# Kernel optimization log

Measured on AMD Instinct MI355X. Metric: run time of the kernel, lower is better.

## Reference

```python
import jax, jax.numpy as jnp
import numpy as np

B = 1024           # number of drug pairs (graphs per side)
ATOMS = 64         # atoms per molecule
N = B * ATOMS      # total atoms per side
H = 512            # hidden_size * number_of_molecules
FFN_H = 2048
OUT = 86           # num_tasks


def setup_inputs() -> dict:
    key = jax.random.key(0)
    ks = jax.random.split(key, 12)
    inv = 1.0 / np.sqrt(H)
    inv2 = 1.0 / np.sqrt(2 * H)
    invf = 1.0 / np.sqrt(FFN_H)
    return {
        "left_output": jax.random.normal(ks[0], (B, H), jnp.float32),
        "right_output": jax.random.normal(ks[1], (B, H), jnp.float32),
        "left_atom": jax.random.normal(ks[2], (N, H), jnp.float32),
        "right_atom": jax.random.normal(ks[3], (N, H), jnp.float32),
        "left_batch": jnp.arange(N, dtype=jnp.int32) // ATOMS,
        "right_batch": jnp.arange(N, dtype=jnp.int32) // ATOMS,
        "noise": jax.random.uniform(ks[4], (B, H), jnp.float32),
        "w_i_w": jax.random.normal(ks[5], (H, H), jnp.float32) * inv,
        "w_i_b": jnp.zeros((H,), jnp.float32),
        "prj_i_w": jax.random.normal(ks[6], (H, H), jnp.float32) * inv,
        "prj_i_b": jnp.zeros((H,), jnp.float32),
        "ffn1_w": jax.random.normal(ks[7], (2 * H, FFN_H), jnp.float32) * inv2,
        "ffn1_b": jnp.zeros((FFN_H,), jnp.float32),
        "ffn2_w": jax.random.normal(ks[8], (FFN_H, OUT), jnp.float32) * invf,
        "ffn2_b": jnp.zeros((OUT,), jnp.float32),
    }


def _seg_softmax(s, seg, num_segments):
    m = jax.ops.segment_max(s, seg, num_segments=num_segments)
    e = jnp.exp(s - m[seg])
    z = jax.ops.segment_sum(e, seg, num_segments=num_segments)
    return e / z[seg]


def reference(left_output, right_output, left_atom, right_atom,
              left_batch, right_batch, noise,
              w_i_w, w_i_b, prj_i_w, prj_i_b,
              ffn1_w, ffn1_b, ffn2_w, ffn2_b):
    # repeat_interleave(left_output, degree(right_batch)) == gather by segment id
    left_align = left_output[right_batch]    # [N_r, H]
    right_align = right_output[left_batch]   # [N_l, H]

    # cross-molecule coattention scores (elementwise product + reduce)
    left_scores = jnp.sum((left_atom @ w_i_w + w_i_b) * (right_align @ prj_i_w + prj_i_b), axis=-1)
    left_scores = _seg_softmax(left_scores, left_batch, B)
    right_scores = jnp.sum((right_atom @ w_i_w + w_i_b) * (left_align @ prj_i_w + prj_i_b), axis=-1)
    right_scores = _seg_softmax(right_scores, right_batch, B)

    # attention-weighted global add pool
    h_output = jax.ops.segment_sum(left_atom * right_align * left_scores[:, None], left_batch, num_segments=B)
    t_output = jax.ops.segment_sum(right_atom * left_align * right_scores[:, None], right_batch, num_segments=B)

    # sign-directed noise perturbation (same noise for both sides, as in original)
    nrm = jnp.maximum(jnp.linalg.norm(noise, axis=-1, keepdims=True), 1e-12)
    noise_n = noise / nrm
    h_pert = h_output + jnp.sign(h_output) * noise_n * 0.1
    t_pert = t_output + jnp.sign(t_output) * noise_n * 0.1

    pair = jnp.concatenate([h_pert, t_pert], axis=-1)  # [B, 2H]
    hid = jax.nn.relu(pair @ ffn1_w + ffn1_b)
    output = hid @ ffn2_w + ffn2_b  # training mode: raw logits, no sigmoid
    return (output, h_output, h_pert, left_scores, right_scores, left_output, right_output)
```

## Files before the change

kernel.cpp:

```cpp
#include <hip/hip_runtime.h>
#include <hip/hip_bf16.h>
#include <float.h>

#define B_ 1024
#define H_ 512
#define N_ (B_ * 64)
#define FFN_ 2048
#define OUT_ 86

typedef __bf16 bf16_t;
typedef __attribute__((ext_vector_type(8))) __bf16 bf16x8;
typedef __attribute__((ext_vector_type(4))) float f32x4;

__device__ __forceinline__ float wred_sum(float v) {
#pragma unroll
  for (int m = 32; m; m >>= 1) v += __shfl_xor(v, m);
  return v;
}

__device__ __forceinline__ void gload_lds16(const void* g, void* l) {
  __builtin_amdgcn_global_load_lds((const __attribute__((address_space(1))) unsigned int*)g,
                                   (__attribute__((address_space(3))) unsigned int*)l, 16, 0, 0);
}

__global__ void k_prep(const float* __restrict__ w_i_b,
                       const float* __restrict__ prj_w, const float* __restrict__ prj_b,
                       float* __restrict__ ev, float* __restrict__ c0) {
  int b = blockIdx.x, l = threadIdx.x;
  float s = 0.f;
  if (b < 512) {
    for (int h = l; h < H_; h += 64) s += prj_w[b * H_ + h] * w_i_b[h];
    s = wred_sum(s);
    if (l == 0) ev[b] = s;
  } else {
    for (int h = l; h < H_; h += 64) s += w_i_b[h] * prj_b[h];
    s = wred_sum(s);
    if (l == 0) c0[0] = s;
  }
}

__global__ void k_cvec(const float* __restrict__ ro, const float* __restrict__ lo,
                       const float* __restrict__ ev, const float* __restrict__ c0,
                       float* __restrict__ cL, float* __restrict__ cR) {
  int b = blockIdx.x, side = blockIdx.y, l = threadIdx.x;
  const float* x = side ? lo : ro;
  float s = 0.f;
  for (int j = l; j < H_; j += 64) s += x[b * H_ + j] * ev[j];
  s = wred_sum(s);
  if (l == 0) (side ? cR : cL)[b] = s + c0[0];
}

template <bool BT, bool BIAS>
__global__ __launch_bounds__(256) void gemm64(const float* __restrict__ A1, const float* __restrict__ A2,
                                              int M1, const float* __restrict__ Bm,
                                              const float* __restrict__ bias, float* __restrict__ C,
                                              int N, int K) {
  __shared__ float As[16][68];
  __shared__ float Bs[16][68];
  const int bm = blockIdx.x * 64, bn = blockIdx.y * 64;
  const float* __restrict__ A = (bm < M1) ? (A1 + (size_t)bm * K) : (A2 + (size_t)(bm - M1) * K);
  const int t = threadIdx.x;
  const int tx = t & 15, ty = t >> 4;
  float acc[4][4] = {};
  for (int k0 = 0; k0 < K; k0 += 16) {
#pragma unroll
    for (int i = 0; i < 4; i++) {
      int m = (t >> 4) + i * 16;
      As[t & 15][m] = A[(size_t)m * K + k0 + (t & 15)];
    }
    if (BT) {
#pragma unroll
      for (int i = 0; i < 4; i++) {
        int n = (t >> 4) + i * 16;
        Bs[t & 15][n] = Bm[(size_t)(bn + n) * K + k0 + (t & 15)];
      }
    } else {
#pragma unroll
      for (int i = 0; i < 4; i++) {
        int kk = (t >> 6) + i * 4;
        Bs[kk][t & 63] = Bm[(size_t)(k0 + kk) * N + bn + (t & 63)];
      }
    }
    __syncthreads();
#pragma unroll
    for (int kk = 0; kk < 16; kk++) {
      float4 av = *(const float4*)&As[kk][ty * 4];
      float4 bv = *(const float4*)&Bs[kk][tx * 4];
      float a_[4] = {av.x, av.y, av.z, av.w};
      float b_[4] = {bv.x, bv.y, bv.z, bv.w};
#pragma unroll
      for (int i = 0; i < 4; i++)
#pragma unroll
        for (int j = 0; j < 4; j++) acc[i][j] += a_[i] * b_[j];
    }
    __syncthreads();
  }
#pragma unroll
  for (int i = 0; i < 4; i++) {
    int m = bm + ty * 4 + i;
    float tmp[4];
#pragma unroll
    for (int j = 0; j < 4; j++) {
      float x = acc[i][j];
      if (BIAS) x += bias[bn + tx * 4 + j];
      tmp[j] = x;
    }
    float4 v;
    v.x = tmp[0]; v.y = tmp[1]; v.z = tmp[2]; v.w = tmp[3];
    *(float4*)&C[(size_t)m * N + bn + tx * 4] = v;
  }
}

__global__ __launch_bounds__(256, 2) void k_atoms2(const float* __restrict__ atomL, const float* __restrict__ atomR,
                                                   const float* __restrict__ uLR,
                                                   const float* __restrict__ cL, const float* __restrict__ cR,
                                                   float* __restrict__ scoresL, float* __restrict__ scoresR,
                                                   float* __restrict__ pL, float* __restrict__ pR) {
  const int gw = blockIdx.x * 4 + (threadIdx.x >> 6);
  const int side = gw >> 10;
  const int b = gw & 1023;
  const int lane = threadIdx.x & 63;

  const float* __restrict__ atom = side ? atomR : atomL;
  const float cb = (side ? cR : cL)[b];
  float* __restrict__ scores = side ? scoresR : scoresL;
  float* __restrict__ p = side ? pR : pL;

  const float* __restrict__ u = uLR + (size_t)gw * H_;
  float ur[8];
  *(f32x4*)&ur[0] = *(const f32x4*)&u[lane * 8];
  *(f32x4*)&ur[4] = *(const f32x4*)&u[lane * 8 + 4];

  const float* __restrict__ base = atom + (size_t)b * 64 * H_ + lane * 8;

  float q[8] = {};
  float m_run = -FLT_MAX, z_run = 0.f;
  float myraw = 0.f;

#pragma unroll
  for (int c = 0; c < 8; c++) {
    float a[8][8];
#pragma unroll
    for (int i = 0; i < 8; i++) {
      const float* rp = base + (size_t)(c * 8 + i) * H_;
      *(f32x4*)&a[i][0] = *(const f32x4*)rp;
      *(f32x4*)&a[i][4] = *(const f32x4*)(rp + 4);
    }
    float d[8];
#pragma unroll
    for (int i = 0; i < 8; i++) {
      float s = 0.f;
#pragma unroll
      for (int j = 0; j < 8; j++) s += a[i][j] * ur[j];
      d[i] = s;
    }
#pragma unroll
    for (int i = 0; i < 8; i++) d[i] = wred_sum(d[i]) + cb;
#pragma unroll
    for (int i = 0; i < 8; i++) myraw = (lane == c * 8 + i) ? d[i] : myraw;
    float mc = d[0];
#pragma unroll
    for (int i = 1; i < 8; i++) mc = fmaxf(mc, d[i]);
    float m_new = fmaxf(m_run, mc);
    float r = __expf(m_run - m_new);
    float e[8];
    float zc = 0.f;
#pragma unroll
    for (int i = 0; i < 8; i++) { e[i] = __expf(d[i] - m_new); zc += e[i]; }
    z_run = z_run * r + zc;
    m_run = m_new;
#pragma unroll
    for (int j = 0; j < 8; j++) q[j] *= r;
#pragma unroll
    for (int i = 0; i < 8; i++)
#pragma unroll
      for (int j = 0; j < 8; j++) q[j] += e[i] * a[i][j];
  }

  const float zinv = 1.f / z_run;
  float outp[8];
#pragma unroll
  for (int j = 0; j < 8; j++) outp[j] = q[j] * zinv;
  float* pd = p + (size_t)b * H_ + lane * 8;
  *(f32x4*)&pd[0] = *(const f32x4*)&outp[0];
  *(f32x4*)&pd[4] = *(const f32x4*)&outp[4];
  scores[(size_t)b * 64 + lane] = __expf(myraw - m_run) * zinv;
}

__global__ __launch_bounds__(512) void k_pert(const float* __restrict__ lo, const float* __restrict__ ro,
                                              const float* __restrict__ noise,
                                              const float* __restrict__ pL, const float* __restrict__ pR,
                                              float* __restrict__ h_out, float* __restrict__ h_pert,
                                              bf16_t* __restrict__ pairbf) {
  const int b = blockIdx.x, t = threadIdx.x;
  float nv = noise[(size_t)b * H_ + t];
  float sq = nv * nv;
  sq = wred_sum(sq);
  __shared__ float red[8];
  if ((t & 63) == 0) red[t >> 6] = sq;
  __syncthreads();
  float tot = 0.f;
#pragma unroll
  for (int i = 0; i < 8; i++) tot += red[i];
  float nrm = fmaxf(sqrtf(tot), 1e-12f);
  float nn = nv / nrm * 0.1f;
  float h = ro[(size_t)b * H_ + t] * pL[(size_t)b * H_ + t];
  float tt = lo[(size_t)b * H_ + t] * pR[(size_t)b * H_ + t];
  float sh = (h > 0.f) ? 1.f : ((h < 0.f) ? -1.f : 0.f);
  float st = (tt > 0.f) ? 1.f : ((tt < 0.f) ? -1.f : 0.f);
  float hp = h + sh * nn;
  float tp = tt + st * nn;
  h_out[(size_t)b * H_ + t] = h;
  h_pert[(size_t)b * H_ + t] = hp;
  pairbf[(size_t)b * 1024 + t] = (bf16_t)hp;
  pairbf[(size_t)b * 1024 + 512 + t] = (bf16_t)tp;
}

__global__ __launch_bounds__(256) void k_w1t(const float* __restrict__ W1, bf16_t* __restrict__ W1t) {
  __shared__ float tile[32][33];
  const int bx = blockIdx.x;
  const int by = blockIdx.y;
  const int tx = threadIdx.x & 31, ty = threadIdx.x >> 5;
#pragma unroll
  for (int i = ty; i < 32; i += 8)
    tile[i][tx] = W1[(size_t)(by * 32 + i) * FFN_ + bx * 32 + tx];
  __syncthreads();
#pragma unroll
  for (int i = ty; i < 32; i += 8)
    W1t[(size_t)(bx * 32 + i) * 1024 + by * 32 + tx] = (bf16_t)tile[tx][i];
}

__global__ __launch_bounds__(256) void k_ffn1(const bf16_t* __restrict__ Abf, const bf16_t* __restrict__ Bt,
                                              const float* __restrict__ bias, float* __restrict__ C) {
  __shared__ bf16_t As[64 * 64];
  __shared__ bf16_t Bs[64 * 64];
  const int bm = blockIdx.x * 64, bn = blockIdx.y * 64;
  const int t = threadIdx.x;
  const int lane = t & 63, wave = t >> 6;
  const int wm = wave & 1, wn = wave >> 1;
  const int l15 = lane & 15, l4 = lane >> 4;
  f32x4 acc[2][2] = {{{0.f, 0.f, 0.f, 0.f}, {0.f, 0.f, 0.f, 0.f}},
                     {{0.f, 0.f, 0.f, 0.f}, {0.f, 0.f, 0.f, 0.f}}};

  for (int k0 = 0; k0 < 1024; k0 += 64) {
#pragma unroll
    for (int r = 0; r < 2; r++) {
      const int off = (r * 256 + t) * 16;
      const int row = off >> 7;
      const int g = (off >> 4) & 7;
      const int scb = ((g ^ (row & 7)) << 4);
      gload_lds16((const char*)Abf + (size_t)(bm + row) * 2048 + k0 * 2 + scb, (char*)As + off);
      gload_lds16((const char*)Bt + (size_t)(bn + row) * 2048 + k0 * 2 + scb, (char*)Bs + off);
    }
    __syncthreads();
#pragma unroll
    for (int ks = 0; ks < 2; ks++) {
      const int ar0 = wm * 32 + l15, ar1 = ar0 + 16;
      const int br0 = wn * 32 + l15, br1 = br0 + 16;
      const int gA = ks * 4 + l4;
      bf16x8 a0 = *(const bf16x8*)((const char*)As + ar0 * 128 + ((gA ^ (ar0 & 7)) << 4));
      bf16x8 a1 = *(const bf16x8*)((const char*)As + ar1 * 128 + ((gA ^ (ar1 & 7)) << 4));
      bf16x8 b0 = *(const bf16x8*)((const char*)Bs + br0 * 128 + ((gA ^ (br0 & 7)) << 4));
      bf16x8 b1 = *(const bf16x8*)((const char*)Bs + br1 * 128 + ((gA ^ (br1 & 7)) << 4));
      acc[0][0] = __builtin_amdgcn_mfma_f32_16x16x32_bf16(a0, b0, acc[0][0], 0, 0, 0);
      acc[0][1] = __builtin_amdgcn_mfma_f32_16x16x32_bf16(a0, b1, acc[0][1], 0, 0, 0);
      acc[1][0] = __builtin_amdgcn_mfma_f32_16x16x32_bf16(a1, b0, acc[1][0], 0, 0, 0);
      acc[1][1] = __builtin_amdgcn_mfma_f32_16x16x32_bf16(a1, b1, acc[1][1], 0, 0, 0);
    }
    __syncthreads();
  }
#pragma unroll
  for (int mi = 0; mi < 2; mi++)
#pragma unroll
    for (int nj = 0; nj < 2; nj++)
#pragma unroll
      for (int r = 0; r < 4; r++) {
        const int m = bm + wm * 32 + mi * 16 + l4 * 4 + r;
        const int n = bn + wn * 32 + nj * 16 + l15;
        float v = acc[mi][nj][r] + bias[n];
        C[(size_t)m * FFN_ + n] = fmaxf(v, 0.f);
      }
}

__global__ void k_w2t(const float* __restrict__ W2, float* __restrict__ W2t) {
  int idx = blockIdx.x * 256 + threadIdx.x;
  if (idx < OUT_ * FFN_) {
    int n = idx / FFN_, k = idx % FFN_;
    W2t[idx] = W2[(size_t)k * OUT_ + n];
  }
}

__global__ __launch_bounds__(256) void k_ffn2(const float* __restrict__ hid, const float* __restrict__ W2t,
                                              const float* __restrict__ b2, float* __restrict__ out) {
  const int b0 = blockIdx.x * 2;
  const int t = threadIdx.x, wave = t >> 6, lane = t & 63;
  float4 h0[8], h1[8];
  const float* r0 = hid + (size_t)b0 * FFN_;
#pragma unroll
  for (int j = 0; j < 8; j++) {
    h0[j] = *(const float4*)&r0[lane * 4 + j * 256];
    h1[j] = *(const float4*)&r0[FFN_ + lane * 4 + j * 256];
  }
  for (int n = wave; n < OUT_; n += 4) {
    const float* wrow = W2t + (size_t)n * FFN_;
    float s0 = 0.f, s1 = 0.f;
#pragma unroll
    for (int j = 0; j < 8; j++) {
      float4 w4 = *(const float4*)&wrow[lane * 4 + j * 256];
      s0 += w4.x * h0[j].x + w4.y * h0[j].y + w4.z * h0[j].z + w4.w * h0[j].w;
      s1 += w4.x * h1[j].x + w4.y * h1[j].y + w4.z * h1[j].z + w4.w * h1[j].w;
    }
    s0 = wred_sum(s0);
    s1 = wred_sum(s1);
    if (lane == 0) {
      out[(size_t)b0 * OUT_ + n] = s0 + b2[n];
      out[(size_t)(b0 + 1) * OUT_ + n] = s1 + b2[n];
    }
  }
}

extern "C" void kernel_launch(void* const* d_in, const int* in_sizes, int n_in,
                              void* d_out, int out_size, void* d_ws, size_t ws_size,
                              hipStream_t stream) {
  const float* lo = (const float*)d_in[0];
  const float* ro = (const float*)d_in[1];
  const float* la = (const float*)d_in[2];
  const float* ra = (const float*)d_in[3];
  const float* noise = (const float*)d_in[6];
  const float* w_i_w = (const float*)d_in[7];
  const float* w_i_b = (const float*)d_in[8];
  const float* prj_w = (const float*)d_in[9];
  const float* prj_b = (const float*)d_in[10];
  const float* W1 = (const float*)d_in[11];
  const float* b1 = (const float*)d_in[12];
  const float* W2 = (const float*)d_in[13];
  const float* b2 = (const float*)d_in[14];

  float* out = (float*)d_out;
  float* o_logits = out;
  float* o_hout  = out + 88064;
  float* o_hpert = o_hout + 524288;
  float* o_ls    = o_hpert + 524288;
  float* o_rs    = o_ls + 65536;
  float* o_lo    = o_rs + 65536;
  float* o_ro    = o_lo + 524288;

  float* ws = (float*)d_ws;
  float* T    = ws; ws += 2048 * 512;
  float* uLR  = ws; ws += 2048 * 512;
  float* pL   = ws; ws += B_ * H_;
  float* pR   = ws; ws += B_ * H_;
  float* hid  = ws; ws += B_ * FFN_;
  float* W2t  = ws; ws += OUT_ * FFN_;
  bf16_t* pairbf = (bf16_t*)ws; ws += B_ * 1024 / 2;
  bf16_t* W1t    = (bf16_t*)ws; ws += FFN_ * 1024 / 2;
  float* ev   = ws; ws += 512;
  float* cL   = ws; ws += 1024;
  float* cR   = ws; ws += 1024;
  float* c0   = ws; ws += 4;

  k_prep<<<513, 64, 0, stream>>>(w_i_b, prj_w, prj_b, ev, c0);
  gemm64<false, true><<<dim3(32, 8), 256, 0, stream>>>(ro, lo, 1024, prj_w, prj_b, T, 512, 512);
  gemm64<true, false><<<dim3(32, 8), 256, 0, stream>>>(T, T, 1 << 30, w_i_w, nullptr, uLR, 512, 512);
  k_cvec<<<dim3(1024, 2), 64, 0, stream>>>(ro, lo, ev, c0, cL, cR);
  k_w1t<<<dim3(64, 32), 256, 0, stream>>>(W1, W1t);
  k_atoms2<<<512, 256, 0, stream>>>(la, ra, uLR, cL, cR, o_ls, o_rs, pL, pR);
  k_pert<<<1024, 512, 0, stream>>>(lo, ro, noise, pL, pR, o_hout, o_hpert, pairbf);
  k_ffn1<<<dim3(16, 32), 256, 0, stream>>>(pairbf, W1t, b1, hid);
  k_w2t<<<688, 256, 0, stream>>>(W2, W2t);
  k_ffn2<<<512, 256, 0, stream>>>(hid, W2t, b2, o_logits);
  hipMemcpyAsync(o_lo, lo, (size_t)B_ * H_ * 4, hipMemcpyDeviceToDevice, stream);
  hipMemcpyAsync(o_ro, ro, (size_t)B_ * H_ * 4, hipMemcpyDeviceToDevice, stream);
}
```

Baseline: 173.3 us.

## Split each molecule's atom attention across four waves with LDS softmax merge

The atom attention kernel now gives each molecule a full 256-thread block, with each of four waves processing 16 atoms instead of one wave handling all 64. Per-wave online-softmax max and sum are merged through shared memory, and the partial pooled vectors are summed in LDS before writing. The aim is more parallelism and more memory-level concurrency when streaming the 268MB of atom data, with fewer registers per thread and a higher occupancy target. In exchange it adds block syncs and LDS traffic for the reduction.

```diff
diff --git a/kernel.cpp b/kernel.cpp
--- a/kernel.cpp
+++ b/kernel.cpp
@@ -111,80 +111,92 @@
   }
 }
 
-__global__ __launch_bounds__(256, 2) void k_atoms2(const float* __restrict__ atomL, const float* __restrict__ atomR,
+__global__ __launch_bounds__(256, 5) void k_atoms3(const float* __restrict__ atomL, const float* __restrict__ atomR,
                                                    const float* __restrict__ uLR,
                                                    const float* __restrict__ cL, const float* __restrict__ cR,
                                                    float* __restrict__ scoresL, float* __restrict__ scoresR,
                                                    float* __restrict__ pL, float* __restrict__ pR) {
-  const int gw = blockIdx.x * 4 + (threadIdx.x >> 6);
-  const int side = gw >> 10;
-  const int b = gw & 1023;
-  const int lane = threadIdx.x & 63;
+  const int bx = blockIdx.x;
+  const int side = bx >> 10, b = bx & 1023;
+  const int t = threadIdx.x, wave = t >> 6, lane = t & 63;
 
   const float* __restrict__ atom = side ? atomR : atomL;
   const float cb = (side ? cR : cL)[b];
   float* __restrict__ scores = side ? scoresR : scoresL;
   float* __restrict__ p = side ? pR : pL;
 
-  const float* __restrict__ u = uLR + (size_t)gw * H_;
+  __shared__ float s_raw[64];
+  __shared__ float mz[4][2];
+  __shared__ float pp[4][512];
+
+  const float* __restrict__ u = uLR + (size_t)bx * H_;
   float ur[8];
   *(f32x4*)&ur[0] = *(const f32x4*)&u[lane * 8];
   *(f32x4*)&ur[4] = *(const f32x4*)&u[lane * 8 + 4];
 
-  const float* __restrict__ base = atom + (size_t)b * 64 * H_ + lane * 8;
+  const float* __restrict__ base = atom + ((size_t)b * 64 + wave * 16) * H_ + lane * 8;
 
   float q[8] = {};
   float m_run = -FLT_MAX, z_run = 0.f;
-  float myraw = 0.f;
-
-#pragma unroll
-  for (int c = 0; c < 8; c++) {
-    float a[8][8];
-#pragma unroll
-    for (int i = 0; i < 8; i++) {
-      const float* rp = base + (size_t)(c * 8 + i) * H_;
+
+#pragma unroll
+  for (int c = 0; c < 4; c++) {
+    float a[4][8];
+#pragma unroll
+    for (int i = 0; i < 4; i++) {
+      const float* rp = base + (size_t)(c * 4 + i) * H_;
       *(f32x4*)&a[i][0] = *(const f32x4*)rp;
       *(f32x4*)&a[i][4] = *(const f32x4*)(rp + 4);
     }
-    float d[8];
-#pragma unroll
-    for (int i = 0; i < 8; i++) {
+    float d[4];
+#pragma unroll
+    for (int i = 0; i < 4; i++) {
       float s = 0.f;
 #pragma unroll
       for (int j = 0; j < 8; j++) s += a[i][j] * ur[j];
       d[i] = s;
     }
 #pragma unroll
-    for (int i = 0; i < 8; i++) d[i] = wred_sum(d[i]) + cb;
-#pragma unroll
-    for (int i = 0; i < 8; i++) myraw = (lane == c * 8 + i) ? d[i] : myraw;
-    float mc = d[0];
-#pragma unroll
-    for (int i = 1; i < 8; i++) mc = fmaxf(mc, d[i]);
+    for (int i = 0; i < 4; i++) d[i] = wred_sum(d[i]) + cb;
+    if (lane == 0) {
+#pragma unroll
+      for (int i = 0; i < 4; i++) s_raw[wave * 16 + c * 4 + i] = d[i];
+    }
+    float mc = fmaxf(fmaxf(d[0], d[1]), fmaxf(d[2], d[3]));
     float m_new = fmaxf(m_run, mc);
     float r = __expf(m_run - m_new);
-    float e[8];
+    float e[4];
     float zc = 0.f;
 #pragma unroll
-    for (int i = 0; i < 8; i++) { e[i] = __expf(d[i] - m_new); zc += e[i]; }
+    for (int i = 0; i < 4; i++) { e[i] = __expf(d[i] - m_new); zc += e[i]; }
     z_run = z_run * r + zc;
     m_run = m_new;
 #pragma unroll
     for (int j = 0; j < 8; j++) q[j] *= r;
 #pragma unroll
-    for (int i = 0; i < 8; i++)
+    for (int i = 0; i < 4; i++)
 #pragma unroll
       for (int j = 0; j < 8; j++) q[j] += e[i] * a[i][j];
   }
 
-  const float zinv = 1.f / z_run;
-  float outp[8];
-#pragma unroll
-  for (int j = 0; j < 8; j++) outp[j] = q[j] * zinv;
-  float* pd = p + (size_t)b * H_ + lane * 8;
-  *(f32x4*)&pd[0] = *(const f32x4*)&outp[0];
-  *(f32x4*)&pd[4] = *(const f32x4*)&outp[4];
-  scores[(size_t)b * 64 + lane] = __expf(myraw - m_run) * zinv;
+  if (lane == 0) { mz[wave][0] = m_run; mz[wave][1] = z_run; }
+  __syncthreads();
+  const float M = fmaxf(fmaxf(mz[0][0], mz[1][0]), fmaxf(mz[2][0], mz[3][0]));
+  const float Z = mz[0][1] * __expf(mz[0][0] - M) + mz[1][1] * __expf(mz[1][0] - M) +
+                  mz[2][1] * __expf(mz[2][0] - M) + mz[3][1] * __expf(mz[3][0] - M);
+  const float f = __expf(m_run - M);
+  float qs[8];
+#pragma unroll
+  for (int j = 0; j < 8; j++) qs[j] = q[j] * f;
+  *(f32x4*)&pp[wave][lane * 8] = *(const f32x4*)&qs[0];
+  *(f32x4*)&pp[wave][lane * 8 + 4] = *(const f32x4*)&qs[4];
+  __syncthreads();
+  const float zinv = 1.f / Z;
+  float v0 = (pp[0][t] + pp[1][t] + pp[2][t] + pp[3][t]) * zinv;
+  float v1 = (pp[0][t + 256] + pp[1][t + 256] + pp[2][t + 256] + pp[3][t + 256]) * zinv;
+  p[(size_t)b * H_ + t] = v0;
+  p[(size_t)b * H_ + t + 256] = v1;
+  if (t < 64) scores[(size_t)b * 64 + t] = __expf(s_raw[t] - M) * zinv;
 }
 
 __global__ __launch_bounds__(512) void k_pert(const float* __restrict__ lo, const float* __restrict__ ro,
@@ -364,7 +376,7 @@
   gemm64<true, false><<<dim3(32, 8), 256, 0, stream>>>(T, T, 1 << 30, w_i_w, nullptr, uLR, 512, 512);
   k_cvec<<<dim3(1024, 2), 64, 0, stream>>>(ro, lo, ev, c0, cL, cR);
   k_w1t<<<dim3(64, 32), 256, 0, stream>>>(W1, W1t);
-  k_atoms2<<<512, 256, 0, stream>>>(la, ra, uLR, cL, cR, o_ls, o_rs, pL, pR);
+  k_atoms3<<<2048, 256, 0, stream>>>(la, ra, uLR, cL, cR, o_ls, o_rs, pL, pR);
   k_pert<<<1024, 512, 0, stream>>>(lo, ro, noise, pL, pR, o_hout, o_hpert, pairbf);
   k_ffn1<<<dim3(16, 32), 256, 0, stream>>>(pairbf, W1t, b1, hid);
   k_w2t<<<688, 256, 0, stream>>>(W2, W2t);
```

Measured after the change: 227.5 us. +31.3%, slower.

## Split each molecule's atom attention across two waves with LDS online-softmax merge

Applied to the files above, without the earlier changes.

The fused score/softmax/pool kernel now gives each graph two wavefronts, each handling 32 of the 64 atoms. The partial max, sum and weighted accumulators are merged through shared memory, and the grid doubles to 1024 blocks. This raises parallelism and memory-level concurrency for the streaming read of the 256 MB of atom data, and it requests higher occupancy. The cost is an extra barrier, shared-memory traffic and a second round of exponentials for the merge.

```diff
diff --git a/kernel.cpp b/kernel.cpp
--- a/kernel.cpp
+++ b/kernel.cpp
@@ -111,34 +111,36 @@
   }
 }
 
-__global__ __launch_bounds__(256, 2) void k_atoms2(const float* __restrict__ atomL, const float* __restrict__ atomR,
+__global__ __launch_bounds__(256, 3) void k_atoms4(const float* __restrict__ atomL, const float* __restrict__ atomR,
                                                    const float* __restrict__ uLR,
                                                    const float* __restrict__ cL, const float* __restrict__ cR,
                                                    float* __restrict__ scoresL, float* __restrict__ scoresR,
                                                    float* __restrict__ pL, float* __restrict__ pR) {
-  const int gw = blockIdx.x * 4 + (threadIdx.x >> 6);
-  const int side = gw >> 10;
-  const int b = gw & 1023;
-  const int lane = threadIdx.x & 63;
+  const int t = threadIdx.x, wave = t >> 6, lane = t & 63;
+  const int pairLocal = wave >> 1;
+  const int half = wave & 1;
+  const int pair = blockIdx.x * 2 + pairLocal;
+  const int side = pair >> 10, b = pair & 1023;
 
   const float* __restrict__ atom = side ? atomR : atomL;
   const float cb = (side ? cR : cL)[b];
-  float* __restrict__ scores = side ? scoresR : scoresL;
-  float* __restrict__ p = side ? pR : pL;
-
-  const float* __restrict__ u = uLR + (size_t)gw * H_;
+
+  __shared__ float s_raw[2][64];
+  __shared__ float mzs[4][2];
+  __shared__ float pp[4][512];
+
+  const float* __restrict__ u = uLR + (size_t)pair * H_;
   float ur[8];
   *(f32x4*)&ur[0] = *(const f32x4*)&u[lane * 8];
   *(f32x4*)&ur[4] = *(const f32x4*)&u[lane * 8 + 4];
 
-  const float* __restrict__ base = atom + (size_t)b * 64 * H_ + lane * 8;
+  const float* __restrict__ base = atom + ((size_t)b * 64 + half * 32) * H_ + lane * 8;
 
   float q[8] = {};
   float m_run = -FLT_MAX, z_run = 0.f;
-  float myraw = 0.f;
-
-#pragma unroll
-  for (int c = 0; c < 8; c++) {
+
+#pragma unroll
+  for (int c = 0; c < 4; c++) {
     float a[8][8];
 #pragma unroll
     for (int i = 0; i < 8; i++) {
@@ -156,8 +158,10 @@
     }
 #pragma unroll
     for (int i = 0; i < 8; i++) d[i] = wred_sum(d[i]) + cb;
-#pragma unroll
-    for (int i = 0; i < 8; i++) myraw = (lane == c * 8 + i) ? d[i] : myraw;
+    if (lane == 0) {
+#pragma unroll
+      for (int i = 0; i < 8; i++) s_raw[pairLocal][half * 32 + c * 8 + i] = d[i];
+    }
     float mc = d[0];
 #pragma unroll
     for (int i = 1; i < 8; i++) mc = fmaxf(mc, d[i]);
@@ -177,14 +181,33 @@
       for (int j = 0; j < 8; j++) q[j] += e[i] * a[i][j];
   }
 
-  const float zinv = 1.f / z_run;
-  float outp[8];
-#pragma unroll
-  for (int j = 0; j < 8; j++) outp[j] = q[j] * zinv;
-  float* pd = p + (size_t)b * H_ + lane * 8;
-  *(f32x4*)&pd[0] = *(const f32x4*)&outp[0];
-  *(f32x4*)&pd[4] = *(const f32x4*)&outp[4];
-  scores[(size_t)b * 64 + lane] = __expf(myraw - m_run) * zinv;
+  if (lane == 0) { mzs[wave][0] = m_run; mzs[wave][1] = z_run; }
+  *(f32x4*)&pp[wave][lane * 8] = *(const f32x4*)&q[0];
+  *(f32x4*)&pp[wave][lane * 8 + 4] = *(const f32x4*)&q[4];
+  __syncthreads();
+
+  const int mp = t >> 7;
+  const int pb = blockIdx.x * 2 + mp;
+  const int sside = pb >> 10, bb = pb & 1023;
+  const float m0 = mzs[mp * 2][0], z0 = mzs[mp * 2][1];
+  const float m1 = mzs[mp * 2 + 1][0], z1 = mzs[mp * 2 + 1][1];
+  const float M = fmaxf(m0, m1);
+  const float f0 = __expf(m0 - M), f1 = __expf(m1 - M);
+  const float zinv = 1.f / (z0 * f0 + z1 * f1);
+  const int col0 = (t & 127) * 4;
+  f32x4 qa = *(const f32x4*)&pp[mp * 2][col0];
+  f32x4 qb = *(const f32x4*)&pp[mp * 2 + 1][col0];
+  f32x4 o;
+  o.x = (qa.x * f0 + qb.x * f1) * zinv;
+  o.y = (qa.y * f0 + qb.y * f1) * zinv;
+  o.z = (qa.z * f0 + qb.z * f1) * zinv;
+  o.w = (qa.w * f0 + qb.w * f1) * zinv;
+  float* pdst = (sside ? pR : pL) + (size_t)bb * H_;
+  *(f32x4*)&pdst[col0] = o;
+  if ((t & 127) < 64) {
+    const int i = t & 63;
+    (sside ? scoresR : scoresL)[(size_t)bb * 64 + i] = __expf(s_raw[mp][i] - M) * zinv;
+  }
 }
 
 __global__ __launch_bounds__(512) void k_pert(const float* __restrict__ lo, const float* __restrict__ ro,
@@ -364,7 +387,7 @@
   gemm64<true, false><<<dim3(32, 8), 256, 0, stream>>>(T, T, 1 << 30, w_i_w, nullptr, uLR, 512, 512);
   k_cvec<<<dim3(1024, 2), 64, 0, stream>>>(ro, lo, ev, c0, cL, cR);
   k_w1t<<<dim3(64, 32), 256, 0, stream>>>(W1, W1t);
-  k_atoms2<<<512, 256, 0, stream>>>(la, ra, uLR, cL, cR, o_ls, o_rs, pL, pR);
+  k_atoms4<<<1024, 256, 0, stream>>>(la, ra, uLR, cL, cR, o_ls, o_rs, pL, pR);
   k_pert<<<1024, 512, 0, stream>>>(lo, ro, noise, pL, pR, o_hout, o_hpert, pairbf);
   k_ffn1<<<dim3(16, 32), 256, 0, stream>>>(pairbf, W1t, b1, hid);
   k_w2t<<<688, 256, 0, stream>>>(W2, W2t);
```

After: 254.0 us. +46.6%, slower.
